# Kernel optimization log

Hardware: AMD Instinct MI355X
Metric: run time of the kernel (lower is better)

The kernel has to match this reference:

```python
import jax, jax.numpy as jnp
import numpy as np

N = 10000      # nodes
S = 4          # num_samples (walks per node)
L = 8          # walk length
F_IN = 128     # in_features == out_features (required by SelfSupervise fc)
H = 128        # out_features (GRU hidden)
ORIG = 64      # original_features
SUB = 100      # self-supervision subsample


def _gru(x, h0, Wih, Whh, bih, bhh):
    """Single-layer unidirectional GRU. x: (L, *batch, F); h0: (*batch, H)."""
    def step(hprev, xt):
        gi = xt @ Wih.T + bih            # (*batch, 3H)
        gh = hprev @ Whh.T + bhh
        ir, iz, inn = jnp.split(gi, 3, axis=-1)
        hr, hz, hn = jnp.split(gh, 3, axis=-1)
        r = jax.nn.sigmoid(ir + hr)
        z = jax.nn.sigmoid(iz + hz)
        n = jnp.tanh(inn + r * hn)
        hnew = (1.0 - z) * n + z * hprev
        return hnew, hnew
    hT, ys = jax.lax.scan(step, h0, x)
    return ys, hT                         # ys: (L, *batch, H), hT: (*batch, H)


def setup_inputs() -> dict:
    key = jax.random.key(0)
    ks = jax.random.split(key, 14)
    s = 0.1  # weight scale for numerical sanity
    return {
        "h":     jax.random.normal(ks[0], (N, F_IN), jnp.float32),
        "y0":    jax.random.uniform(ks[1], (N, ORIG), jnp.float32),  # binary-ish targets in [0,1]
        "Wih_w": s * jax.random.normal(ks[2], (3 * H, L), jnp.float32),
        "Whh_w": s * jax.random.normal(ks[3], (3 * H, H), jnp.float32),
        "bih_w": s * jax.random.normal(ks[4], (3 * H,), jnp.float32),
        "bhh_w": s * jax.random.normal(ks[5], (3 * H,), jnp.float32),
        "Wih":   s * jax.random.normal(ks[6], (3 * H, F_IN + H), jnp.float32),
        "Whh":   s * jax.random.normal(ks[7], (3 * H, H), jnp.float32),
        "bih":   s * jax.random.normal(ks[8], (3 * H,), jnp.float32),
        "bhh":   s * jax.random.normal(ks[9], (3 * H,), jnp.float32),
        "W_ss":  s * jax.random.normal(ks[10], (ORIG, F_IN), jnp.float32),
        "b_ss":  s * jax.random.normal(ks[11], (ORIG,), jnp.float32),
        "walks": jax.random.randint(ks[12], (S, N, L), 0, N),
        "idxs":  jax.random.randint(ks[13], (SUB,), 0, N),
    }


def reference(h, y0, Wih_w, Whh_w, bih_w, bhh_w, Wih, Whh, bih, bhh, W_ss, b_ss, walks, idxs):
    # uniqueness: index of first occurrence of each node within its walk, in [0, L)
    uniq = jnp.argmax(walks[..., :, None] == walks[..., None, :], axis=-1)  # (S, N, L)
    walks_f = jnp.flip(walks, axis=-1)
    uniq_f = jnp.flip(uniq, axis=-1)
    u1h = jax.nn.one_hot(uniq_f, L, dtype=h.dtype)          # (S, N, L, L)

    hw = jnp.take(h, walks_f, axis=0)                       # (S, N, L, F_IN) gather

    h0 = jnp.zeros((S, N, H), dtype=h.dtype)
    x_walk = jnp.moveaxis(u1h, -2, 0)                       # (L, S, N, L)
    y_walk, h_walk = _gru(x_walk, h0, Wih_w, Whh_w, bih_w, bhh_w)  # (L,S,N,H), (S,N,H)
    # torch: h_walk.mean(0, keepdim=True) over layer dim of size 1 -> identity

    x_main = jnp.concatenate([jnp.moveaxis(hw, -2, 0), y_walk], axis=-1)  # (L, S, N, F_IN+H)
    y_seq, hT = _gru(x_main, h_walk, Wih, Whh, bih, bhh)    # (L,S,N,H), (S,N,H)
    y = jnp.moveaxis(y_seq, 0, -2)                          # (S, N, L, H)

    # self-supervision: subsample nodes, next-step BCE
    y_t = jnp.take(y0, walks_f, axis=0)[:, idxs, 1:, :]     # (S, SUB, L-1, ORIG)
    y_hat = y[:, idxs, :-1, :] @ W_ss.T + b_ss              # (S, SUB, L-1, ORIG)
    pos_w = 1.0 / jnp.mean(y_t)
    loss = jnp.mean(pos_w * y_t * jax.nn.softplus(-y_hat)
                    + (1.0 - y_t) * jax.nn.softplus(y_hat))

    # torch: h.mean(0) over layer dim of size 1 -> hT; activation = Identity; dropout = eval
    return hT, loss
```

## Files before the change

### kernel.cpp

```cpp
#include <hip/hip_runtime.h>
#include <math.h>

#define NN    10000
#define SSS   4
#define LL    8
#define HH    128
#define NSEQ  40000
#define SUBN  100
#define ORIGF 64
#define TA    512

#define FATB  768
#define FATQ  (FATB * 48)
#define TAILB ((NSEQ - FATQ) / 16)
#define GRID  (FATB + TAILB)

typedef unsigned short u16;
typedef short bf16x8 __attribute__((ext_vector_type(8)));
typedef float f32x4 __attribute__((ext_vector_type(4)));

#define L2E 1.4426950408889634f

#define WL_OFF    0
#define BWRZ_OFF  6144
#define BWIN_OFF  7168
#define BWHN_OFF  7680
#define BMRZ_OFF  8192
#define BMIN_OFF  9216
#define BMHN_OFF  9728
#define HB_OFF    10240
#define HB_STR    128
#define HBBUF     2048
#define HB_SSTR   4096
#define XB_OFF    34816
#define XB_STR    128
#define XB_SSTR   16384
#define SWF_OFF   133120
#define SUF_OFF   134656
#define SCNT_OFF  136192
#define SANY_OFF  136384
#define WSSA_ROWS 24
#define WSSA_OFF  WL_OFF
#define WSSB_OFF  136448
#define RED_OFF   136448
#define LDS_TOTAL 163072

#define WB_BYTE_OFF 64
#define W_HHW_N 49152
#define W_HH_N  49152
#define W_IH_N  98304
#define W_TOTAL (W_HHW_N + W_HH_N + W_IH_N)
#define WS_NEED ((size_t)WB_BYTE_OFF + (size_t)W_TOTAL * 2 + (size_t)NN * HH * 2)

__device__ __forceinline__ float bf2f(u16 u) {
  return __uint_as_float(((unsigned)u) << 16);
}
__device__ __forceinline__ u16 f2bf(float f) {
  unsigned u = __float_as_uint(f);
  u += 0x7fffu + ((u >> 16) & 1u);
  return (u16)(u >> 16);
}
__device__ __forceinline__ bf16x8 pack8(float4 v0, float4 v1) {
  bf16x8 r;
  r[0] = (short)f2bf(v0.x); r[1] = (short)f2bf(v0.y);
  r[2] = (short)f2bf(v0.z); r[3] = (short)f2bf(v0.w);
  r[4] = (short)f2bf(v1.x); r[5] = (short)f2bf(v1.y);
  r[6] = (short)f2bf(v1.z); r[7] = (short)f2bf(v1.w);
  return r;
}
__device__ __forceinline__ float sig2_(float xs) {
  return __builtin_amdgcn_rcpf(1.f + __builtin_amdgcn_exp2f(-xs));
}
__device__ __forceinline__ float tanh2_(float xs) {
  return 1.f - 2.f * __builtin_amdgcn_rcpf(__builtin_amdgcn_exp2f(xs) + 1.f);
}
__device__ __forceinline__ float softplusf_(float x) {
  return fmaxf(x, 0.f) + log1pf(__expf(-fabsf(x)));
}

__global__ void k_zero(float* ws) {
  if (threadIdx.x < 4) ws[threadIdx.x] = 0.f;
}

__global__ void k_prep(const float* __restrict__ whhw, const float* __restrict__ whh,
                       const float* __restrict__ wih, float* __restrict__ ws) {
  const int i = blockIdx.x * 256 + threadIdx.x;
  u16* wb = (u16*)((char*)ws + WB_BYTE_OFF);
  if (i < W_HHW_N) {
    const int row = i >> 7;
    wb[i] = f2bf(whhw[i] * ((row < 256) ? L2E : 2.f * L2E));
  } else if (i < W_HHW_N + W_HH_N) {
    const int j = i - W_HHW_N, row = j >> 7;
    wb[i] = f2bf(whh[j] * ((row < 256) ? L2E : 2.f * L2E));
  } else {
    const int j = i - W_HHW_N - W_HH_N, row = j >> 8;
    wb[i] = f2bf(wih[j] * ((row < 256) ? L2E : 2.f * L2E));
  }
}

__global__ void k_prep_h(const float* __restrict__ h, float* __restrict__ ws) {
  const int i = blockIdx.x * 256 + threadIdx.x;
  u16* hb16 = (u16*)((char*)ws + WB_BYTE_OFF) + W_TOTAL;
  hb16[i] = f2bf(h[i]);
}

template<bool BF, int NSS>
__device__ __forceinline__ void rum_body(
    const int q0,
    const float* __restrict__ hfeat, const float* __restrict__ y0,
    const float* __restrict__ WihW,  const float* __restrict__ bihW,
    const float* __restrict__ bhhW,
    const float* __restrict__ bih,   const float* __restrict__ bhh,
    const float* __restrict__ W_ss,  const float* __restrict__ b_ss,
    const int* __restrict__ walks,   const int* __restrict__ idxs,
    float* __restrict__ out, float* __restrict__ ws)
{
  constexpr int MAS = 16 * NSS;
  extern __shared__ char sm[];
  u16*   WLb  = (u16*)(sm + WL_OFF);
  float* bwrz = (float*)(sm + BWRZ_OFF);
  float* bwin = (float*)(sm + BWIN_OFF);
  float* bwhn = (float*)(sm + BWHN_OFF);
  float* bmrz = (float*)(sm + BMRZ_OFF);
  float* bmin = (float*)(sm + BMIN_OFF);
  float* bmhn = (float*)(sm + BMHN_OFF);
  u16*   hb   = (u16*)(sm + HB_OFF);
  u16*   xb   = (u16*)(sm + XB_OFF);
  int*   swf  = (int*)(sm + SWF_OFF);
  int*   suf  = (int*)(sm + SUF_OFF);
  int*   scnt = (int*)(sm + SCNT_OFF);
  int*   sany = (int*)(sm + SANY_OFF);

  const u16* wb     = (const u16*)((const char*)ws + WB_BYTE_OFF);
  const u16* whhw_b = wb;
  const u16* whh_b  = wb + W_HHW_N;
  const u16* wih_b  = wb + W_HHW_N + W_HH_N;
  const u16* hf16   = wb + W_TOTAL;

  const int tid = threadIdx.x;
  const int lane = tid & 63, c = lane & 15, qd = lane >> 4;
  const int wv = tid >> 6;
  const int i0 = wv * 16 + c;

  if (tid < MAS) {
    const int m = tid;
    scnt[m] = 0;
    const int q = q0 + m;
    int w[LL];
    #pragma unroll
    for (int l = 0; l < LL; ++l) w[l] = walks[q * LL + l];
    #pragma unroll
    for (int l = 0; l < LL; ++l) {
      int u = l;
      #pragma unroll
      for (int l2 = LL - 1; l2 >= 0; --l2) if (w[l2] == w[l]) u = l2;
      swf[m * LL + (LL - 1 - l)] = w[l];
      suf[m * LL + (LL - 1 - l)] = u;
    }
  }
  if (tid == 0) *sany = 0;
  for (int idx = tid; idx < 3072; idx += TA)
    WLb[idx] = f2bf(WihW[idx] * ((idx < 2048) ? L2E : 2.f * L2E));
  if (tid < 256) {
    bwrz[tid] = (bihW[tid] + bhhW[tid]) * L2E;
    bmrz[tid] = (bih[tid] + bhh[tid]) * L2E;
  }
  if (tid < 128) {
    bwin[tid] = 2.f * L2E * bihW[256 + tid]; bwhn[tid] = 2.f * L2E * bhhW[256 + tid];
    bmin[tid] = 2.f * L2E * bih[256 + tid];  bmhn[tid] = 2.f * L2E * bhh[256 + tid];
  }
  __syncthreads();

  for (int p = tid; p < MAS * SUBN; p += TA) {
    const int m = p / SUBN, i = p % SUBN;
    if (idxs[i] == (q0 + m) % NN) { atomicAdd(&scnt[m], 1); *sany = 1; }
  }

  const float bw1 = bwrz[i0], bw2 = bwrz[HH + i0], bw3 = bwin[i0], bw4 = bwhn[i0];
  const float bm1 = bmrz[i0], bm2 = bmrz[HH + i0], bm3 = bmin[i0], bm4 = bmhn[i0];

  float hreg[NSS][4];
  #pragma unroll
  for (int s = 0; s < NSS; ++s)
    #pragma unroll
    for (int r2 = 0; r2 < 4; ++r2) hreg[s][r2] = 0.f;

  {
    bf16x8 BA[3][4];
    #pragma unroll
    for (int tl = 0; tl < 3; ++tl) {
      const int row = (tl * 8 + wv) * 16 + c;
      #pragma unroll
      for (int k = 0; k < 4; ++k)
        BA[tl][k] = *(const bf16x8*)(whhw_b + row * HH + k * 32 + qd * 8);
    }
    #pragma unroll 2
    for (int t = 0; t < LL; ++t) {
      #pragma unroll
      for (int s = 0; s < NSS; ++s) {
        f32x4 D[3];
        #pragma unroll
        for (int tl = 0; tl < 3; ++tl) D[tl] = (f32x4){0.f, 0.f, 0.f, 0.f};
        if (t > 0) {
          const u16* hbc = hb + s * HB_SSTR + (t & 1) * HBBUF;
          bf16x8 a[4];
          #pragma unroll
          for (int k = 0; k < 4; ++k)
            a[k] = *(const bf16x8*)(hbc + c * HB_STR + (((4 * k + qd) ^ c) << 3));
          #pragma unroll
          for (int tl = 0; tl < 3; ++tl) {
            f32x4 d = D[tl];
            #pragma unroll
            for (int k = 0; k < 4; ++k)
              d = __builtin_amdgcn_mfma_f32_16x16x32_bf16(a[k], BA[tl][k], d, 0, 0, 0);
            D[tl] = d;
          }
        }
        u16* hbn = hb + s * HB_SSTR + ((t + 1) & 1) * HBBUF;
        u16* xbs = xb + s * XB_SSTR;
        #pragma unroll
        for (int reg = 0; reg < 4; ++reg) {
          const int ml = qd * 4 + reg;
          const int u = suf[(s * 16 + ml) * LL + t];
          const float r = sig2_(bf2f(WLb[i0 * LL + u]) + D[0][reg] + bw1);
          const float z = sig2_(bf2f(WLb[(HH + i0) * LL + u]) + D[1][reg] + bw2);
          const float n = tanh2_(bf2f(WLb[(2 * HH + i0) * LL + u]) + bw3
                                 + r * (D[2][reg] + bw4));
          const float hn = n + z * (hreg[s][reg] - n);
          hreg[s][reg] = hn;
          const u16 hv = f2bf(hn);
          const int slot = (((i0 >> 3) ^ ml) << 3) + (i0 & 7);
          hbn[ml * HB_STR + slot] = hv;
          xbs[(t * 16 + ml) * XB_STR + slot] = hv;
        }
      }
      __syncthreads();
    }
  }

  const bool anyf = (*sany != 0);

  if (anyf) {
    if (tid < ORIGF) ((float*)(sm + BWHN_OFF))[tid] = b_ss[tid];
    for (int idx = tid; idx < HH * ORIGF; idx += TA) {
      const int kc = idx & 127, o = idx >> 7;
      float* dst = (kc < WSSA_ROWS)
          ? (float*)(sm + WSSA_OFF + kc * 256)
          : (float*)(sm + WSSB_OFF + (kc - WSSA_ROWS) * 256);
      dst[o] = W_ss[o * HH + kc];
    }
  }

  bf16x8 BW[3][8], BC[3][4];
  #pragma unroll
  for (int tl = 0; tl < 3; ++tl) {
    const int row = (tl * 8 + wv) * 16 + c;
    #pragma unroll
    for (int kk = 0; kk < 8; ++kk)
      BW[tl][kk] = *(const bf16x8*)(wih_b + row * 256 + kk * 32 + qd * 8);
    #pragma unroll
    for (int k = 0; k < 4; ++k)
      BC[tl][k] = *(const bf16x8*)(whh_b + row * HH + k * 32 + qd * 8);
  }

  float pAcc = 0.f, pBcc = 0.f, pScc = 0.f;

  #pragma unroll 2
  for (int t = 0; t < LL; ++t) {
    #pragma unroll
    for (int s = 0; s < NSS; ++s) {
      const int node = swf[(s * 16 + c) * LL + t];
      bf16x8 ah[4];
      if constexpr (BF) {
        const u16* hp = hf16 + (size_t)node * HH + qd * 8;
        #pragma unroll
        for (int k = 0; k < 4; ++k) ah[k] = *(const bf16x8*)(hp + k * 32);
      } else {
        const float* hp = hfeat + (size_t)node * HH + qd * 8;
        #pragma unroll
        for (int k = 0; k < 4; ++k)
          ah[k] = pack8(*(const float4*)(hp + k * 32),
                        *(const float4*)(hp + k * 32 + 4));
      }
      const u16* xbs = xb + s * XB_SSTR + t * 16 * XB_STR;
      bf16x8 ay[4];
      #pragma unroll
      for (int k = 0; k < 4; ++k)
        ay[k] = *(const bf16x8*)(xbs + c * XB_STR + (((4 * k + qd) ^ c) << 3));
      const u16* hbc = hb + s * HB_SSTR + (t & 1) * HBBUF;
      bf16x8 a[4];
      #pragma unroll
      for (int k = 0; k < 4; ++k)
        a[k] = *(const bf16x8*)(hbc + c * HB_STR + (((4 * k + qd) ^ c) << 3));

      f32x4 Drz[2], Dnr, Dni;
      #pragma unroll
      for (int tl = 0; tl < 2; ++tl) {
        f32x4 d = {0.f, 0.f, 0.f, 0.f};
        #pragma unroll
        for (int k = 0; k < 4; ++k)
          d = __builtin_amdgcn_mfma_f32_16x16x32_bf16(a[k], BC[tl][k], d, 0, 0, 0);
        #pragma unroll
        for (int k = 0; k < 4; ++k)
          d = __builtin_amdgcn_mfma_f32_16x16x32_bf16(ah[k], BW[tl][k], d, 0, 0, 0);
        #pragma unroll
        for (int k = 0; k < 4; ++k)
          d = __builtin_amdgcn_mfma_f32_16x16x32_bf16(ay[k], BW[tl][4 + k], d, 0, 0, 0);
        Drz[tl] = d;
      }
      {
        f32x4 dr = {0.f, 0.f, 0.f, 0.f}, di = {0.f, 0.f, 0.f, 0.f};
        #pragma unroll
        for (int k = 0; k < 4; ++k)
          dr = __builtin_amdgcn_mfma_f32_16x16x32_bf16(a[k], BC[2][k], dr, 0, 0, 0);
        #pragma unroll
        for (int k = 0; k < 4; ++k)
          di = __builtin_amdgcn_mfma_f32_16x16x32_bf16(ah[k], BW[2][k], di, 0, 0, 0);
        #pragma unroll
        for (int k = 0; k < 4; ++k)
          di = __builtin_amdgcn_mfma_f32_16x16x32_bf16(ay[k], BW[2][4 + k], di, 0, 0, 0);
        Dnr = dr; Dni = di;
      }
      u16* hbn = hb + s * HB_SSTR + ((t + 1) & 1) * HBBUF;
      #pragma unroll
      for (int reg = 0; reg < 4; ++reg) {
        const int ml = qd * 4 + reg;
        const float r = sig2_(Drz[0][reg] + bm1);
        const float z = sig2_(Drz[1][reg] + bm2);
        const float n = tanh2_(Dni[reg] + bm3 + r * (Dnr[reg] + bm4));
        const float hn = n + z * (hreg[s][reg] - n);
        hreg[s][reg] = hn;
        hbn[ml * HB_STR + (((i0 >> 3) ^ ml) << 3) + (i0 & 7)] = f2bf(hn);
      }
    }

    if (t < LL - 1 && anyf) {
      __syncthreads();
      const float* bssl = (const float*)(sm + BWHN_OFF);
      for (int idx = tid; idx < MAS * ORIGF; idx += TA) {
        const int m = idx >> 6, o = idx & 63;
        const int cnt = scnt[m];
        if (cnt > 0) {
          const int ml = m & 15;
          const u16* hrow = hb + (m >> 4) * HB_SSTR + ((t + 1) & 1) * HBBUF
                          + ml * HB_STR;
          const float fc = (float)cnt;
          const float yt = y0[(size_t)swf[m * LL + t + 1] * ORIGF + o];
          float a0 = bssl[o], a1 = 0.f, a2 = 0.f, a3 = 0.f;
          #pragma unroll 1
          for (int kc8 = 0; kc8 < 16; ++kc8) {
            const bf16x8 xv = *(const bf16x8*)(hrow + ((kc8 ^ ml) << 3));
            const int kc = kc8 * 8;
            const char* wbase = (kc < WSSA_ROWS)
                ? (sm + WSSA_OFF + kc * 256)
                : (sm + WSSB_OFF + (kc - WSSA_ROWS) * 256);
            a0 = fmaf(((const float*)(wbase))[o],          bf2f((u16)xv[0]), a0);
            a1 = fmaf(((const float*)(wbase + 256))[o],    bf2f((u16)xv[1]), a1);
            a2 = fmaf(((const float*)(wbase + 512))[o],    bf2f((u16)xv[2]), a2);
            a3 = fmaf(((const float*)(wbase + 768))[o],    bf2f((u16)xv[3]), a3);
            a0 = fmaf(((const float*)(wbase + 1024))[o],   bf2f((u16)xv[4]), a0);
            a1 = fmaf(((const float*)(wbase + 1280))[o],   bf2f((u16)xv[5]), a1);
            a2 = fmaf(((const float*)(wbase + 1536))[o],   bf2f((u16)xv[6]), a2);
            a3 = fmaf(((const float*)(wbase + 1792))[o],   bf2f((u16)xv[7]), a3);
          }
          const float acc = (a0 + a1) + (a2 + a3);
          const float sp = softplusf_(-acc);
          pAcc += fc * yt * sp;
          pBcc += fc * (1.f - yt) * (sp + acc);
          pScc += fc * yt;
        }
      }
    }
    __syncthreads();
  }

  #pragma unroll
  for (int s = 0; s < NSS; ++s)
    #pragma unroll
    for (int reg = 0; reg < 4; ++reg)
      out[(size_t)(q0 + s * 16 + qd * 4 + reg) * HH + i0] = hreg[s][reg];

  if (anyf) {
    float* red = (float*)(sm + RED_OFF);
    red[tid] = pAcc; red[TA + tid] = pBcc; red[2 * TA + tid] = pScc;
    __syncthreads();
    if (wv == 0) {
      float a = 0.f, b = 0.f, s = 0.f;
      for (int k2 = lane; k2 < TA; k2 += 64) {
        a += red[k2]; b += red[TA + k2]; s += red[2 * TA + k2];
      }
      #pragma unroll
      for (int off = 32; off > 0; off >>= 1) {
        a += __shfl_down(a, off); b += __shfl_down(b, off); s += __shfl_down(s, off);
      }
      if (lane == 0) {
        atomicAdd(&ws[1], a); atomicAdd(&ws[2], b); atomicAdd(&ws[3], s);
      }
    }
  }
}

template<bool BF>
__global__ __launch_bounds__(TA, 2) void k_rum(
    const float* __restrict__ hfeat, const float* __restrict__ y0,
    const float* __restrict__ WihW,  const float* __restrict__ bihW,
    const float* __restrict__ bhhW,
    const float* __restrict__ bih,   const float* __restrict__ bhh,
    const float* __restrict__ W_ss,  const float* __restrict__ b_ss,
    const int* __restrict__ walks,   const int* __restrict__ idxs,
    float* __restrict__ out, float* __restrict__ ws)
{
  const int b = blockIdx.x;
  if (b < FATB) {
    rum_body<BF, 3>(b * 48, hfeat, y0, WihW, bihW, bhhW, bih, bhh,
                    W_ss, b_ss, walks, idxs, out, ws);
  } else {
    rum_body<BF, 1>(FATQ + (b - FATB) * 16, hfeat, y0, WihW, bihW, bhhW,
                    bih, bhh, W_ss, b_ss, walks, idxs, out, ws);
  }
}

__global__ void k_final(const float* __restrict__ ws, float* __restrict__ out) {
  if (threadIdx.x == 0) {
    const float cnt = (float)(SSS * SUBN * (LL - 1) * ORIGF);
    const float pos_w = cnt / ws[3];
    const float loss = (pos_w * ws[1] + ws[2]) / cnt;
    out[NSEQ * HH] = loss;
  }
}

extern "C" void kernel_launch(void* const* d_in, const int* in_sizes, int n_in,
                              void* d_out, int out_size, void* d_ws, size_t ws_size,
                              hipStream_t stream) {
  const float* hfeat = (const float*)d_in[0];
  const float* y0    = (const float*)d_in[1];
  const float* Wih_w = (const float*)d_in[2];
  const float* Whh_w = (const float*)d_in[3];
  const float* bih_w = (const float*)d_in[4];
  const float* bhh_w = (const float*)d_in[5];
  const float* Wih   = (const float*)d_in[6];
  const float* Whh   = (const float*)d_in[7];
  const float* bih   = (const float*)d_in[8];
  const float* bhh   = (const float*)d_in[9];
  const float* W_ss  = (const float*)d_in[10];
  const float* b_ss  = (const float*)d_in[11];
  const int* walks = (const int*)d_in[12];
  const int* idxs  = (const int*)d_in[13];
  float* out = (float*)d_out;
  float* ws = (float*)d_ws;

  const bool bf = (ws_size >= WS_NEED);

  (void)hipFuncSetAttribute((const void*)k_rum<true>,
                            hipFuncAttributeMaxDynamicSharedMemorySize, LDS_TOTAL);
  (void)hipFuncSetAttribute((const void*)k_rum<false>,
                            hipFuncAttributeMaxDynamicSharedMemorySize, LDS_TOTAL);

  k_zero<<<1, 64, 0, stream>>>(ws);
  k_prep<<<W_TOTAL / 256, 256, 0, stream>>>(Whh_w, Whh, Wih, ws);
  if (bf) k_prep_h<<<(NN * HH) / 256, 256, 0, stream>>>(hfeat, ws);

  if (bf)
    k_rum<true><<<GRID, TA, LDS_TOTAL, stream>>>(hfeat, y0, Wih_w, bih_w, bhh_w,
                                                 bih, bhh, W_ss, b_ss,
                                                 walks, idxs, out, ws);
  else
    k_rum<false><<<GRID, TA, LDS_TOTAL, stream>>>(hfeat, y0, Wih_w, bih_w, bhh_w,
                                                  bih, bhh, W_ss, b_ss,
                                                  walks, idxs, out, ws);

  k_final<<<1, 64, 0, stream>>>(ws, out);
}
```

Before: 374.9 us.

## Add low-LDS GRU kernel spilling walk-GRU outputs to global workspace

Adds a new fused GRU kernel with 80 sequences per block. It writes the walk-GRU hidden outputs to a bf16 global workspace buffer instead of keeping them in LDS, which cuts shared memory per block to about 89 KB so two blocks can fit per CU. The main GRU then reads those outputs back from global memory as MFMA operands. The kernel is used only when the workspace is large enough; otherwise the old path runs. The cost is extra global write and read traffic, plus a dependence on the workspace size.

After: 404.6 us. +7.9%, slower.

```diff
diff --git a/kernel.cpp b/kernel.cpp
--- a/kernel.cpp
+++ b/kernel.cpp
@@ -14,6 +14,9 @@
 #define FATQ  (FATB * 48)
 #define TAILB ((NSEQ - FATQ) / 16)
 #define GRID  (FATB + TAILB)
+
+#define MA5   80
+#define GRID5 (NSEQ / MA5)
 
 typedef unsigned short u16;
 typedef short bf16x8 __attribute__((ext_vector_type(8)));
@@ -45,12 +48,22 @@
 #define RED_OFF   136448
 #define LDS_TOTAL 163072
 
+#define Q_HB_OFF   10240
+#define Q_SWF_OFF  51200
+#define Q_SUF_OFF  53760
+#define Q_SCNT_OFF 56320
+#define Q_SANY_OFF 56640
+#define Q_WSS_OFF  56704
+#define Q_RED_OFF  56704
+#define Q_LDS      89472
+
 #define WB_BYTE_OFF 64
 #define W_HHW_N 49152
 #define W_HH_N  49152
 #define W_IH_N  98304
 #define W_TOTAL (W_HHW_N + W_HH_N + W_IH_N)
-#define WS_NEED ((size_t)WB_BYTE_OFF + (size_t)W_TOTAL * 2 + (size_t)NN * HH * 2)
+#define WS_NEED  ((size_t)WB_BYTE_OFF + (size_t)W_TOTAL * 2 + (size_t)NN * HH * 2)
+#define WS_NEED2 (WS_NEED + (size_t)NSEQ * LL * HH * 2)
 
 __device__ __forceinline__ float bf2f(u16 u) {
   return __uint_as_float(((unsigned)u) << 16);
@@ -102,6 +115,284 @@
   const int i = blockIdx.x * 256 + threadIdx.x;
   u16* hb16 = (u16*)((char*)ws + WB_BYTE_OFF) + W_TOTAL;
   hb16[i] = f2bf(h[i]);
+}
+
+__global__ __launch_bounds__(TA, 2) void k_rum5(
+    const float* __restrict__ y0,
+    const float* __restrict__ WihW,  const float* __restrict__ bihW,
+    const float* __restrict__ bhhW,
+    const float* __restrict__ bih,   const float* __restrict__ bhh,
+    const float* __restrict__ W_ss,  const float* __restrict__ b_ss,
+    const int* __restrict__ walks,   const int* __restrict__ idxs,
+    float* __restrict__ out, float* __restrict__ ws)
+{
+  constexpr int NSS = 5, MAS = MA5;
+  extern __shared__ char sm[];
+  u16*   WLb  = (u16*)(sm + WL_OFF);
+  float* bwrz = (float*)(sm + BWRZ_OFF);
+  float* bwin = (float*)(sm + BWIN_OFF);
+  float* bwhn = (float*)(sm + BWHN_OFF);
+  float* bmrz = (float*)(sm + BMRZ_OFF);
+  float* bmin = (float*)(sm + BMIN_OFF);
+  float* bmhn = (float*)(sm + BMHN_OFF);
+  u16*   hb   = (u16*)(sm + Q_HB_OFF);
+  int*   swf  = (int*)(sm + Q_SWF_OFF);
+  int*   suf  = (int*)(sm + Q_SUF_OFF);
+  int*   scnt = (int*)(sm + Q_SCNT_OFF);
+  int*   sany = (int*)(sm + Q_SANY_OFF);
+
+  const u16* wb     = (const u16*)((const char*)ws + WB_BYTE_OFF);
+  const u16* whhw_b = wb;
+  const u16* whh_b  = wb + W_HHW_N;
+  const u16* wih_b  = wb + W_HHW_N + W_HH_N;
+  const u16* hf16   = wb + W_TOTAL;
+  u16*       ywg    = (u16*)((char*)ws + WB_BYTE_OFF) + W_TOTAL + NN * HH;
+
+  const int tid = threadIdx.x;
+  const int lane = tid & 63, c = lane & 15, qd = lane >> 4;
+  const int wv = tid >> 6;
+  const int i0 = wv * 16 + c;
+  const int q0 = blockIdx.x * MAS;
+
+  if (tid < MAS) {
+    const int m = tid;
+    scnt[m] = 0;
+    const int q = q0 + m;
+    int w[LL];
+    #pragma unroll
+    for (int l = 0; l < LL; ++l) w[l] = walks[q * LL + l];
+    #pragma unroll
+    for (int l = 0; l < LL; ++l) {
+      int u = l;
+      #pragma unroll
+      for (int l2 = LL - 1; l2 >= 0; --l2) if (w[l2] == w[l]) u = l2;
+      swf[m * LL + (LL - 1 - l)] = w[l];
+      suf[m * LL + (LL - 1 - l)] = u;
+    }
+  }
+  if (tid == 0) *sany = 0;
+  for (int idx = tid; idx < 3072; idx += TA)
+    WLb[idx] = f2bf(WihW[idx] * ((idx < 2048) ? L2E : 2.f * L2E));
+  if (tid < 256) {
+    bwrz[tid] = (bihW[tid] + bhhW[tid]) * L2E;
+    bmrz[tid] = (bih[tid] + bhh[tid]) * L2E;
+  }
+  if (tid < 128) {
+    bwin[tid] = 2.f * L2E * bihW[256 + tid]; bwhn[tid] = 2.f * L2E * bhhW[256 + tid];
+    bmin[tid] = 2.f * L2E * bih[256 + tid];  bmhn[tid] = 2.f * L2E * bhh[256 + tid];
+  }
+  __syncthreads();
+
+  for (int p = tid; p < MAS * SUBN; p += TA) {
+    const int m = p / SUBN, i = p % SUBN;
+    if (idxs[i] == (q0 + m) % NN) { atomicAdd(&scnt[m], 1); *sany = 1; }
+  }
+
+  const float bw1 = bwrz[i0], bw2 = bwrz[HH + i0], bw3 = bwin[i0], bw4 = bwhn[i0];
+  const float bm1 = bmrz[i0], bm2 = bmrz[HH + i0], bm3 = bmin[i0], bm4 = bmhn[i0];
+
+  float hreg[NSS][4];
+  #pragma unroll
+  for (int s = 0; s < NSS; ++s)
+    #pragma unroll
+    for (int r2 = 0; r2 < 4; ++r2) hreg[s][r2] = 0.f;
+
+  {
+    bf16x8 BA[3][4];
+    #pragma unroll
+    for (int tl = 0; tl < 3; ++tl) {
+      const int row = (tl * 8 + wv) * 16 + c;
+      #pragma unroll
+      for (int k = 0; k < 4; ++k)
+        BA[tl][k] = *(const bf16x8*)(whhw_b + row * HH + k * 32 + qd * 8);
+    }
+    #pragma unroll 1
+    for (int t = 0; t < LL; ++t) {
+      #pragma unroll
+      for (int s = 0; s < NSS; ++s) {
+        f32x4 D[3];
+        #pragma unroll
+        for (int tl = 0; tl < 3; ++tl) D[tl] = (f32x4){0.f, 0.f, 0.f, 0.f};
+        if (t > 0) {
+          const u16* hbc = hb + s * HB_SSTR + (t & 1) * HBBUF;
+          bf16x8 a[4];
+          #pragma unroll
+          for (int k = 0; k < 4; ++k)
+            a[k] = *(const bf16x8*)(hbc + c * HB_STR + (((4 * k + qd) ^ c) << 3));
+          #pragma unroll
+          for (int tl = 0; tl < 3; ++tl) {
+            f32x4 d = D[tl];
+            #pragma unroll
+            for (int k = 0; k < 4; ++k)
+              d = __builtin_amdgcn_mfma_f32_16x16x32_bf16(a[k], BA[tl][k], d, 0, 0, 0);
+            D[tl] = d;
+          }
+        }
+        u16* hbn = hb + s * HB_SSTR + ((t + 1) & 1) * HBBUF;
+        #pragma unroll
+        for (int reg = 0; reg < 4; ++reg) {
+          const int ml = qd * 4 + reg;
+          const int u = suf[(s * 16 + ml) * LL + t];
+          const float r = sig2_(bf2f(WLb[i0 * LL + u]) + D[0][reg] + bw1);
+          const float z = sig2_(bf2f(WLb[(HH + i0) * LL + u]) + D[1][reg] + bw2);
+          const float n = tanh2_(bf2f(WLb[(2 * HH + i0) * LL + u]) + bw3
+                                 + r * (D[2][reg] + bw4));
+          const float hn = n + z * (hreg[s][reg] - n);
+          hreg[s][reg] = hn;
+          const u16 hv = f2bf(hn);
+          hbn[ml * HB_STR + (((i0 >> 3) ^ ml) << 3) + (i0 & 7)] = hv;
+          ywg[((size_t)(q0 + s * 16 + ml) * LL + t) * HH + i0] = hv;
+        }
+      }
+      __syncthreads();
+    }
+  }
+
+  const bool anyf = (*sany != 0);
+
+  if (anyf) {
+    if (tid < ORIGF) ((float*)(sm + BWHN_OFF))[tid] = b_ss[tid];
+    for (int idx = tid; idx < HH * ORIGF; idx += TA) {
+      const int kc = idx & 127, o = idx >> 7;
+      ((float*)(sm + Q_WSS_OFF + kc * 256))[o] = W_ss[o * HH + kc];
+    }
+  }
+
+  bf16x8 BW[3][8], BC[3][4];
+  #pragma unroll
+  for (int tl = 0; tl < 3; ++tl) {
+    const int row = (tl * 8 + wv) * 16 + c;
+    #pragma unroll
+    for (int kk = 0; kk < 8; ++kk)
+      BW[tl][kk] = *(const bf16x8*)(wih_b + row * 256 + kk * 32 + qd * 8);
+    #pragma unroll
+    for (int k = 0; k < 4; ++k)
+      BC[tl][k] = *(const bf16x8*)(whh_b + row * HH + k * 32 + qd * 8);
+  }
+
+  float pAcc = 0.f, pBcc = 0.f, pScc = 0.f;
+
+  #pragma unroll 1
+  for (int t = 0; t < LL; ++t) {
+    #pragma unroll
+    for (int s = 0; s < NSS; ++s) {
+      const int node = swf[(s * 16 + c) * LL + t];
+      const u16* hp = hf16 + (size_t)node * HH + qd * 8;
+      bf16x8 ah[4];
+      #pragma unroll
+      for (int k = 0; k < 4; ++k) ah[k] = *(const bf16x8*)(hp + k * 32);
+      const u16* yp = ywg + ((size_t)(q0 + s * 16 + c) * LL + t) * HH + qd * 8;
+      bf16x8 ay[4];
+      #pragma unroll
+      for (int k = 0; k < 4; ++k) ay[k] = *(const bf16x8*)(yp + k * 32);
+      const u16* hbc = hb + s * HB_SSTR + (t & 1) * HBBUF;
+      bf16x8 a[4];
+      #pragma unroll
+      for (int k = 0; k < 4; ++k)
+        a[k] = *(const bf16x8*)(hbc + c * HB_STR + (((4 * k + qd) ^ c) << 3));
+
+      f32x4 Drz[2], Dnr, Dni;
+      #pragma unroll
+      for (int tl = 0; tl < 2; ++tl) {
+        f32x4 d = {0.f, 0.f, 0.f, 0.f};
+        #pragma unroll
+        for (int k = 0; k < 4; ++k)
+          d = __builtin_amdgcn_mfma_f32_16x16x32_bf16(a[k], BC[tl][k], d, 0, 0, 0);
+        #pragma unroll
+        for (int k = 0; k < 4; ++k)
+          d = __builtin_amdgcn_mfma_f32_16x16x32_bf16(ah[k], BW[tl][k], d, 0, 0, 0);
+        #pragma unroll
+        for (int k = 0; k < 4; ++k)
+          d = __builtin_amdgcn_mfma_f32_16x16x32_bf16(ay[k], BW[tl][4 + k], d, 0, 0, 0);
+        Drz[tl] = d;
+      }
+      {
+        f32x4 dr = {0.f, 0.f, 0.f, 0.f}, di = {0.f, 0.f, 0.f, 0.f};
+        #pragma unroll
+        for (int k = 0; k < 4; ++k)
+          dr = __builtin_amdgcn_mfma_f32_16x16x32_bf16(a[k], BC[2][k], dr, 0, 0, 0);
+        #pragma unroll
+        for (int k = 0; k < 4; ++k)
+          di = __builtin_amdgcn_mfma_f32_16x16x32_bf16(ah[k], BW[2][k], di, 0, 0, 0);
+        #pragma unroll
+        for (int k = 0; k < 4; ++k)
+          di = __builtin_amdgcn_mfma_f32_16x16x32_bf16(ay[k], BW[2][4 + k], di, 0, 0, 0);
+        Dnr = dr; Dni = di;
+      }
+      u16* hbn = hb + s * HB_SSTR + ((t + 1) & 1) * HBBUF;
+      #pragma unroll
+      for (int reg = 0; reg < 4; ++reg) {
+        const int ml = qd * 4 + reg;
+        const float r = sig2_(Drz[0][reg] + bm1);
+        const float z = sig2_(Drz[1][reg] + bm2);
+        const float n = tanh2_(Dni[reg] + bm3 + r * (Dnr[reg] + bm4));
+        const float hn = n + z * (hreg[s][reg] - n);
+        hreg[s][reg] = hn;
+        hbn[ml * HB_STR + (((i0 >> 3) ^ ml) << 3) + (i0 & 7)] = f2bf(hn);
+      }
+    }
+
+    if (t < LL - 1 && anyf) {
+      __syncthreads();
+      const float* bssl = (const float*)(sm + BWHN_OFF);
+      for (int idx = tid; idx < MAS * ORIGF; idx += TA) {
+        const int m = idx >> 6, o = idx & 63;
+        const int cnt = scnt[m];
+        if (cnt > 0) {
+          const int ml = m & 15;
+          const u16* hrow = hb + (m >> 4) * HB_SSTR + ((t + 1) & 1) * HBBUF
+                          + ml * HB_STR;
+          const float fc = (float)cnt;
+          const float yt = y0[(size_t)swf[m * LL + t + 1] * ORIGF + o];
+          float a0 = bssl[o], a1 = 0.f, a2 = 0.f, a3 = 0.f;
+          #pragma unroll 1
+          for (int kc8 = 0; kc8 < 16; ++kc8) {
+            const bf16x8 xv = *(const bf16x8*)(hrow + ((kc8 ^ ml) << 3));
+            const char* wbase = sm + Q_WSS_OFF + kc8 * 2048;
+            a0 = fmaf(((const float*)(wbase))[o],        bf2f((u16)xv[0]), a0);
+            a1 = fmaf(((const float*)(wbase + 256))[o],  bf2f((u16)xv[1]), a1);
+            a2 = fmaf(((const float*)(wbase + 512))[o],  bf2f((u16)xv[2]), a2);
+            a3 = fmaf(((const float*)(wbase + 768))[o],  bf2f((u16)xv[3]), a3);
+            a0 = fmaf(((const float*)(wbase + 1024))[o], bf2f((u16)xv[4]), a0);
+            a1 = fmaf(((const float*)(wbase + 1280))[o], bf2f((u16)xv[5]), a1);
+            a2 = fmaf(((const float*)(wbase + 1536))[o], bf2f((u16)xv[6]), a2);
+            a3 = fmaf(((const float*)(wbase + 1792))[o], bf2f((u16)xv[7]), a3);
+          }
+          const float acc = (a0 + a1) + (a2 + a3);
+          const float sp = softplusf_(-acc);
+          pAcc += fc * yt * sp;
+          pBcc += fc * (1.f - yt) * (sp + acc);
+          pScc += fc * yt;
+        }
+      }
+    }
+    __syncthreads();
+  }
+
+  #pragma unroll
+  for (int s = 0; s < NSS; ++s)
+    #pragma unroll
+    for (int reg = 0; reg < 4; ++reg)
+      out[(size_t)(q0 + s * 16 + qd * 4 + reg) * HH + i0] = hreg[s][reg];
+
+  if (anyf) {
+    float* red = (float*)(sm + Q_RED_OFF);
+    red[tid] = pAcc; red[TA + tid] = pBcc; red[2 * TA + tid] = pScc;
+    __syncthreads();
+    if (wv == 0) {
+      float a = 0.f, b = 0.f, s = 0.f;
+      for (int k2 = lane; k2 < TA; k2 += 64) {
+        a += red[k2]; b += red[TA + k2]; s += red[2 * TA + k2];
+      }
+      #pragma unroll
+      for (int off = 32; off > 0; off >>= 1) {
+        a += __shfl_down(a, off); b += __shfl_down(b, off); s += __shfl_down(s, off);
+      }
+      if (lane == 0) {
+        atomicAdd(&ws[1], a); atomicAdd(&ws[2], b); atomicAdd(&ws[3], s);
+      }
+    }
+  }
 }
 
 template<bool BF, int NSS>
@@ -354,14 +645,14 @@
             const char* wbase = (kc < WSSA_ROWS)
                 ? (sm + WSSA_OFF + kc * 256)
                 : (sm + WSSB_OFF + (kc - WSSA_ROWS) * 256);
-            a0 = fmaf(((const float*)(wbase))[o],          bf2f((u16)xv[0]), a0);
-            a1 = fmaf(((const float*)(wbase + 256))[o],    bf2f((u16)xv[1]), a1);
-            a2 = fmaf(((const float*)(wbase + 512))[o],    bf2f((u16)xv[2]), a2);
-            a3 = fmaf(((const float*)(wbase + 768))[o],    bf2f((u16)xv[3]), a3);
-            a0 = fmaf(((const float*)(wbase + 1024))[o],   bf2f((u16)xv[4]), a0);
-            a1 = fmaf(((const float*)(wbase + 1280))[o],   bf2f((u16)xv[5]), a1);
-            a2 = fmaf(((const float*)(wbase + 1536))[o],   bf2f((u16)xv[6]), a2);
-            a3 = fmaf(((const float*)(wbase + 1792))[o],   bf2f((u16)xv[7]), a3);
+            a0 = fmaf(((const float*)(wbase))[o],        bf2f((u16)xv[0]), a0);
+            a1 = fmaf(((const float*)(wbase + 256))[o],  bf2f((u16)xv[1]), a1);
+            a2 = fmaf(((const float*)(wbase + 512))[o],  bf2f((u16)xv[2]), a2);
+            a3 = fmaf(((const float*)(wbase + 768))[o],  bf2f((u16)xv[3]), a3);
+            a0 = fmaf(((const float*)(wbase + 1024))[o], bf2f((u16)xv[4]), a0);
+            a1 = fmaf(((const float*)(wbase + 1280))[o], bf2f((u16)xv[5]), a1);
+            a2 = fmaf(((const float*)(wbase + 1536))[o], bf2f((u16)xv[6]), a2);
+            a3 = fmaf(((const float*)(wbase + 1792))[o], bf2f((u16)xv[7]), a3);
           }
           const float acc = (a0 + a1) + (a2 + a3);
           const float sp = softplusf_(-acc);
@@ -449,8 +740,11 @@
   float* out = (float*)d_out;
   float* ws = (float*)d_ws;
 
-  const bool bf = (ws_size >= WS_NEED);
-
+  const bool bf  = (ws_size >= WS_NEED);
+  const bool big = (ws_size >= WS_NEED2);
+
+  (void)hipFuncSetAttribute((const void*)k_rum5,
+                            hipFuncAttributeMaxDynamicSharedMemorySize, Q_LDS);
   (void)hipFuncSetAttribute((const void*)k_rum<true>,
                             hipFuncAttributeMaxDynamicSharedMemorySize, LDS_TOTAL);
   (void)hipFuncSetAttribute((const void*)k_rum<false>,
@@ -460,14 +754,19 @@
   k_prep<<<W_TOTAL / 256, 256, 0, stream>>>(Whh_w, Whh, Wih, ws);
   if (bf) k_prep_h<<<(NN * HH) / 256, 256, 0, stream>>>(hfeat, ws);
 
-  if (bf)
+  if (bf && big) {
+    k_rum5<<<GRID5, TA, Q_LDS, stream>>>(y0, Wih_w, bih_w, bhh_w,
+                                         bih, bhh, W_ss, b_ss,
+                                         walks, idxs, out, ws);
+  } else if (bf) {
     k_rum<true><<<GRID, TA, LDS_TOTAL, stream>>>(hfeat, y0, Wih_w, bih_w, bhh_w,
                                                  bih, bhh, W_ss, b_ss,
                                                  walks, idxs, out, ws);
-  else
+  } else {
     k_rum<false><<<GRID, TA, LDS_TOTAL, stream>>>(hfeat, y0, Wih_w, bih_w, bhh_w,
                                                   bih, bhh, W_ss, b_ss,
                                                   walks, idxs, out, ws);
+  }
 
   k_final<<<1, 64, 0, stream>>>(ws, out);
 }
```
